# Kernel optimization log

Measured on AMD Instinct MI355X. Metric: run time of the kernel, lower is better.

Reference implementation:

```python
import jax, jax.numpy as jnp
import numpy as np

TOKEN = 40      # half window -> token_len D = 81
STRIDE = 4
NHEAD = 9
EPS = 1e-5
NEG = -1e30


def _tokenize(x):
    # x: [B, L] -> [B, S, D] centered sliding windows, zero padded
    B, L = x.shape
    D = 2 * TOKEN + 1
    S = -(-L // STRIDE)
    xp = jnp.pad(x, ((0, 0), (TOKEN, TOKEN)))
    idx = jnp.arange(S)[:, None] * STRIDE + jnp.arange(D)[None, :]
    return xp[:, idx]


def _pe(S, D):
    pos = jnp.arange(S, dtype=jnp.float32)[:, None]
    div = jnp.exp(-jnp.log(jnp.float32(10000.0)) * jnp.arange(0, D, 2, dtype=jnp.float32) / D)
    ang = pos * div  # [S, ceil(D/2)]
    pe = jnp.zeros((S, D), dtype=jnp.float32)
    pe = pe.at[:, 0::2].set(jnp.sin(ang))
    pe = pe.at[:, 1::2].set(jnp.cos(ang[:, : D // 2]))
    return pe


def _bn(x, g, b, axes):
    # training-mode batch norm over `axes`, channels last
    m = x.mean(axes, keepdims=True)
    v = x.var(axes, keepdims=True)
    return (x - m) / jnp.sqrt(v + EPS) * g + b


def _forward(x, basel, cali_spec, Wq, Wk, Wq2, Wk2, Wv2, Cv, Wo1, Wo2,
             corr_weight, h_weight, corr_map, g1, b1, ff1_w, ff1_b, g2, b2,
             ff2_w, ff2_b, g3, b3, token_v_w, token_v_b, beta1, alpha1, alpha2,
             fc1_w, fc1_b, bnf1_g, bnf1_b, fc2_w, fc2_b, bnf2_g, bnf2_b, fc3_w, fc3_b):
    D = 2 * TOKEN + 1
    dk = D // NHEAD
    # data normalization (load_data_scale semantics)
    xm = jnp.min(x[:, 20:-20])
    xs = jnp.abs(jnp.max(x[:, 20:-20] - xm))
    xn = (x - xm) / xs
    bs = basel[:, ::STRIDE]                      # [B, S]
    tx = _tokenize(xn)                           # [B, S, D]
    B, S, _ = tx.shape
    pe = _pe(S, D)
    tx = tx + pe
    cn = (cali_spec - xm) / xs
    tc = _tokenize(cn) + pe                      # [Bc, S, D]
    Bc = tc.shape[0]

    # ---- branch 2: calibration-spectrum attention over the batch dim ----
    Q2 = jnp.einsum('bse,hed->shbd', tx, Wq2)    # [S,H,B,dk]
    K2 = jnp.einsum('bse,hed->shbd', tx, Wk2)
    V2 = jnp.einsum('bse,hed->shbd', tx, Wv2)
    cK = jnp.einsum('cse,hed->shcd', tc, Wk2)    # [S,H,Bc,dk]
    cV = jnp.einsum('cse,hed->shcd', tc, Wv2)
    Kc = jnp.concatenate([K2, cK], axis=2)       # [S,H,B+Bc,dk]
    Vc = jnp.concatenate([V2, cV], axis=2)
    sc = jnp.einsum('shbd,shkd->shbk', Q2, Kc) / jnp.sqrt(jnp.float32(dk))
    cols = jnp.arange(B + Bc)
    # banded mask: each sample sees only itself among batch columns, all cali columns
    mask = (cols[None, :] >= B) | (cols[None, :] == jnp.arange(B)[:, None])  # [B, B+Bc]
    sc = jnp.where(mask[None, None], sc, NEG)
    A2 = jax.nn.softmax(sc, axis=-1)
    h2 = jnp.einsum('shbk,shkd->bshd', A2, Vc).reshape(B, S, D) @ Wo2  # [B,S,D]

    # ---- branch 1: correlation-map-biased attention over spectral positions ----
    xh = tx + h2
    Qs = jnp.einsum('bse,hed->bhsd', xh, Wq)
    Ks = jnp.einsum('bse,hed->bhsd', xh, Wk)
    Vs = jnp.einsum('bse,hed->bhsd', xh, Wq)     # original uses Wq for V (bug preserved)
    cw = corr_weight[0]
    bias = (corr_map @ Cv) / jnp.sqrt(jnp.float32(S))  # band_num == S
    As = (1.0 - cw) * jnp.einsum('bhsd,bhtd->bhst', Qs, Ks) / jnp.sqrt(jnp.float32(dk)) + cw * bias
    As = jax.nn.softmax(As, axis=-1)
    h1 = jnp.einsum('bhst,bhtd->bshd', As, Vs).reshape(B, S, D) @ Wo1
    hw = h_weight[0]
    att = (1.0 - hw) * h1 + hw * h2

    # ---- SpectrA residual + FF (BatchNorm over channels) ----
    ma = _bn(att + tx, g1, b1, (0, 1))
    f = jax.nn.relu(ma @ ff1_w + ff1_b)
    f = _bn(f, g2, b2, (0, 1))
    f = jax.nn.relu(f @ ff2_w + ff2_b)
    res = _bn(ma + f, g3, b3, (0, 1))

    # ---- ACiNet head ----
    a = (res @ token_v_w + token_v_b) * jax.nn.softmax(res @ beta1, axis=-1)
    a = a.sum(-1)                                # [B, S]
    fea = alpha1[0] * a + alpha2[0] * bs
    h = jax.nn.relu(fea @ fc1_w + fc1_b)
    h = _bn(h, bnf1_g, bnf1_b, (0,))
    h = jax.nn.relu(h @ fc2_w + fc2_b)
    h = _bn(h, bnf2_g, bnf2_b, (0,))
    return jnp.tanh(h @ fc3_w + fc3_b)


def setup_inputs() -> dict:
    key = jax.random.key(0)
    ks = iter(jax.random.split(key, 64))
    def rn(shape, s=0.05):
        return jax.random.normal(next(ks), shape, dtype=jnp.float32) * s
    B, Bc, L = 32, 16, 2048
    D, H, dk, S, FF, FC1, FC2, Y = 81, 9, 9, 512, 256, 512, 256, 4
    f32 = jnp.float32
    return {
        'x': rn((B, L), 1.0), 'basel': rn((B, L), 1.0), 'cali_spec': rn((Bc, L), 1.0),
        'Wq': rn((H, D, dk)), 'Wk': rn((H, D, dk)), 'Wq2': rn((H, D, dk)),
        'Wk2': rn((H, D, dk)), 'Wv2': rn((H, D, dk)),
        'Cv': rn((S, S)), 'Wo1': rn((D, D)), 'Wo2': rn((D, D)),
        'corr_weight': jnp.array([0.2], dtype=f32), 'h_weight': jnp.array([0.8], dtype=f32),
        'corr_map': rn((S, S), 1.0),
        'g1': jnp.ones(D, f32), 'b1': jnp.zeros(D, f32),
        'ff1_w': rn((D, FF)), 'ff1_b': jnp.zeros(FF, f32),
        'g2': jnp.ones(FF, f32), 'b2': jnp.zeros(FF, f32),
        'ff2_w': rn((FF, D)), 'ff2_b': jnp.zeros(D, f32),
        'g3': jnp.ones(D, f32), 'b3': jnp.zeros(D, f32),
        'token_v_w': rn((D, D)), 'token_v_b': jnp.zeros(D, f32),
        'beta1': jnp.ones((D, D), f32),
        'alpha1': jnp.array([0.8], dtype=f32), 'alpha2': jnp.array([0.2], dtype=f32),
        'fc1_w': rn((S, FC1)), 'fc1_b': jnp.zeros(FC1, f32),
        'bnf1_g': jnp.ones(FC1, f32), 'bnf1_b': jnp.zeros(FC1, f32),
        'fc2_w': rn((FC1, FC2)), 'fc2_b': jnp.zeros(FC2, f32),
        'bnf2_g': jnp.ones(FC2, f32), 'bnf2_b': jnp.zeros(FC2, f32),
        'fc3_w': rn((FC2, Y)), 'fc3_b': jnp.zeros(Y, f32),
    }


def reference(x, basel, cali_spec, Wq, Wk, Wq2, Wk2, Wv2, Cv, Wo1, Wo2,
              corr_weight, h_weight, corr_map, g1, b1, ff1_w, ff1_b, g2, b2,
              ff2_w, ff2_b, g3, b3, token_v_w, token_v_b, beta1, alpha1, alpha2,
              fc1_w, fc1_b, bnf1_g, bnf1_b, fc2_w, fc2_b, bnf2_g, bnf2_b, fc3_w, fc3_b):
    return _forward(x, basel, cali_spec, Wq, Wk, Wq2, Wk2, Wv2, Cv, Wo1, Wo2,
                    corr_weight, h_weight, corr_map, g1, b1, ff1_w, ff1_b, g2, b2,
                    ff2_w, ff2_b, g3, b3, token_v_w, token_v_b, beta1, alpha1, alpha2,
                    fc1_w, fc1_b, bnf1_g, bnf1_b, fc2_w, fc2_b, bnf2_g, bnf2_b, fc3_w, fc3_b)
```

## Files before the change

kernel.cpp:

```cpp
#include <hip/hip_runtime.h>
#include <hip/hip_bf16.h>
#include <math.h>

#define EPSV 1e-5f

typedef float vf4 __attribute__((ext_vector_type(4)));


__global__ void minmax_part(const float* __restrict__ x, float* __restrict__ part) {
    __shared__ float smin[256], smax[256];
    int tid = threadIdx.x;
    float mn = 1e30f, mx = -1e30f;
    for (int i = blockIdx.x * 256 + tid; i < 32 * 2008; i += 64 * 256) {
        int b = i / 2008, c = i % 2008 + 20;
        float v = x[b * 2048 + c];
        mn = fminf(mn, v); mx = fmaxf(mx, v);
    }
    smin[tid] = mn; smax[tid] = mx; __syncthreads();
    for (int off = 128; off > 0; off >>= 1) {
        if (tid < off) { smin[tid] = fminf(smin[tid], smin[tid + off]); smax[tid] = fmaxf(smax[tid], smax[tid + off]); }
        __syncthreads();
    }
    if (tid == 0) { part[blockIdx.x] = smin[0]; part[64 + blockIdx.x] = smax[0]; }
}

__global__ void minmax_fin(const float* __restrict__ part, float* __restrict__ scal) {
    __shared__ float smn[64], smx[64];
    int tid = threadIdx.x;
    smn[tid] = part[tid]; smx[tid] = part[64 + tid]; __syncthreads();
    for (int off = 32; off > 0; off >>= 1) {
        if (tid < off) { smn[tid] = fminf(smn[tid], smn[tid + off]); smx[tid] = fmaxf(smx[tid], smx[tid + off]); }
        __syncthreads();
    }
    if (tid == 0) { scal[0] = smn[0]; scal[1] = smx[0] - smn[0]; }
}

__global__ void pe_kernel(float* __restrict__ pe) {
    int idx = blockIdx.x * blockDim.x + threadIdx.x;
    if (idx >= 512 * 81) return;
    int d = idx % 81, s = idx / 81;
    int j = d >> 1;
    float dv = __expf(-9.210340371976184f * (2.0f * (float)j) / 81.0f);
    float ang = (float)s * dv;
    pe[idx] = (d & 1) ? cosf(ang) : sinf(ang);
}

__global__ void tokenize_kernel(const float* __restrict__ x, const float* __restrict__ cali,
                                const float* __restrict__ scal, const float* __restrict__ pe,
                                float* __restrict__ txall) {
    int idx = blockIdx.x * blockDim.x + threadIdx.x;
    if (idx >= 48 * 512 * 81) return;
    int d = idx % 81;
    int s = (idx / 81) % 512;
    int r = idx / (81 * 512);
    float xm = scal[0], inv_xs = 1.0f / scal[1];
    int oc = s * 4 + d - 40;
    float val = 0.0f;
    if (oc >= 0 && oc < 2048) {
        float sv = (r < 32) ? x[r * 2048 + oc] : cali[(r - 32) * 2048 + oc];
        val = (sv - xm) * inv_xs;
    }
    txall[idx] = val + pe[s * 81 + d];
}


__global__ __launch_bounds__(256) void qkv2_kernel(const float* __restrict__ txall,
                            const float* __restrict__ Wq2, const float* __restrict__ Wk2,
                            const float* __restrict__ Wv2,
                            float* __restrict__ Q2, float* __restrict__ Kc, float* __restrict__ Vc) {
    __shared__ float rows_[64 * 84];
    __shared__ float Wl[84 * 84];
    int blk = blockIdx.x;
    int t, rb;
    if (blk < 256)      { t = 0; rb = blk; }
    else if (blk < 640) { t = 1; rb = blk - 256; }
    else                { t = 2; rb = blk - 640; }
    int row0 = rb * 64;
    int k = row0 >> 9;
    int s0 = row0 & 511;
    const float* W = (t == 0) ? Wq2 : (t == 1) ? Wk2 : Wv2;
    int tid = threadIdx.x;
    for (int i = tid; i < 64 * 84; i += 256) {
        int c = i % 84;
        rows_[i] = (c < 81) ? txall[(row0 + i / 84) * 81 + c] : 0.0f;
    }
    for (int i = tid; i < 84 * 84; i += 256) {
        int e = i / 84, hd = i % 84;
        Wl[i] = (e < 81 && hd < 81) ? W[(hd / 9) * 729 + e * 9 + (hd % 9)] : 0.0f;
    }
    __syncthreads();
    for (int o = tid; o < 336; o += 256) {
        int r4 = o / 21, cg = o % 21;
        int c0 = cg * 4;
        const float* rp = rows_ + r4 * 4 * 84;
        vf4 acc0 = 0.0f, acc1 = 0.0f, acc2 = 0.0f, acc3 = 0.0f;
        #pragma unroll 7
        for (int e = 0; e < 84; e += 4) {
            vf4 w0 = *(const vf4*)(Wl + (e + 0) * 84 + c0);
            vf4 w1 = *(const vf4*)(Wl + (e + 1) * 84 + c0);
            vf4 w2 = *(const vf4*)(Wl + (e + 2) * 84 + c0);
            vf4 w3 = *(const vf4*)(Wl + (e + 3) * 84 + c0);
            vf4 r0 = *(const vf4*)(rp + e);
            vf4 r1 = *(const vf4*)(rp + 84 + e);
            vf4 r2 = *(const vf4*)(rp + 168 + e);
            vf4 r3 = *(const vf4*)(rp + 252 + e);
            acc0 += r0[0] * w0 + r0[1] * w1 + r0[2] * w2 + r0[3] * w3;
            acc1 += r1[0] * w0 + r1[1] * w1 + r1[2] * w2 + r1[3] * w3;
            acc2 += r2[0] * w0 + r2[1] * w1 + r2[2] * w2 + r2[3] * w3;
            acc3 += r3[0] * w0 + r3[1] * w1 + r3[2] * w2 + r3[3] * w3;
        }
        vf4 av[4] = {acc0, acc1, acc2, acc3};
        #pragma unroll
        for (int cc = 0; cc < 4; cc++) {
            int col = c0 + cc;
            if (col < 81) {
                int h = col / 9, d = col % 9;
                #pragma unroll
                for (int rr = 0; rr < 4; rr++) {
                    int s = s0 + r4 * 4 + rr;
                    if (t == 0)      Q2[((s * 9 + h) * 32 + k) * 9 + d] = av[rr][cc];
                    else if (t == 1) Kc[((s * 9 + h) * 48 + k) * 9 + d] = av[rr][cc];
                    else             Vc[((s * 9 + h) * 48 + k) * 9 + d] = av[rr][cc];
                }
            }
        }
    }
}

__global__ void attn2_kernel(const float* __restrict__ Q2, const float* __restrict__ Kc,
                             const float* __restrict__ Vc, float* __restrict__ tmp2) {
    int tid = blockIdx.x * blockDim.x + threadIdx.x;
    if (tid >= 512 * 9 * 32) return;
    int b = tid & 31;
    int h = (tid >> 5) % 9;
    int s = tid / 288;
    const float* q = Q2 + ((s * 9 + h) * 32 + b) * 9;
    float qr[9];
    #pragma unroll
    for (int d = 0; d < 9; d++) qr[d] = q[d] * (1.0f / 3.0f);
    const float* Kb = Kc + (s * 9 + h) * 48 * 9;
    const float* Vb = Vc + (s * 9 + h) * 48 * 9;
    float l = 0.0f, outv[9];
    #pragma unroll
    for (int d = 0; d < 9; d++) outv[d] = 0.0f;
    #pragma unroll
    for (int j = 0; j < 17; j++) {
        int k = (j == 0) ? b : 31 + j;
        const float* kp = Kb + k * 9;
        float acc = 0.0f;
        #pragma unroll
        for (int d = 0; d < 9; d++) acc += qr[d] * kp[d];
        float p = __expf(acc);
        l += p;
        const float* vp = Vb + k * 9;
        #pragma unroll
        for (int d = 0; d < 9; d++) outv[d] += p * vp[d];
    }
    float invl = 1.0f / l;
    float* op = tmp2 + (b * 512 + s) * 81 + h * 9;
    #pragma unroll
    for (int d = 0; d < 9; d++) op[d] = outv[d] * invl;
}

__global__ __launch_bounds__(256) void h2xh_kernel(const float* __restrict__ tmp2,
                            const float* __restrict__ Wo2, const float* __restrict__ txall,
                            float* __restrict__ h2, float* __restrict__ xh) {
    __shared__ float rows_[64 * 84];
    __shared__ float Wl[84 * 84];
    int row0 = blockIdx.x * 64;
    int tid = threadIdx.x;
    for (int i = tid; i < 64 * 84; i += 256) {
        int c = i % 84;
        rows_[i] = (c < 81) ? tmp2[(row0 + i / 84) * 81 + c] : 0.0f;
    }
    for (int i = tid; i < 84 * 84; i += 256) {
        int e = i / 84, c = i % 84;
        Wl[i] = (e < 81 && c < 81) ? Wo2[e * 81 + c] : 0.0f;
    }
    __syncthreads();
    for (int o = tid; o < 336; o += 256) {
        int r4 = o / 21, cg = o % 21;
        int c0 = cg * 4;
        const float* rp = rows_ + r4 * 4 * 84;
        vf4 acc0 = 0.0f, acc1 = 0.0f, acc2 = 0.0f, acc3 = 0.0f;
        #pragma unroll 7
        for (int e = 0; e < 84; e += 4) {
            vf4 w0 = *(const vf4*)(Wl + (e + 0) * 84 + c0);
            vf4 w1 = *(const vf4*)(Wl + (e + 1) * 84 + c0);
            vf4 w2 = *(const vf4*)(Wl + (e + 2) * 84 + c0);
            vf4 w3 = *(const vf4*)(Wl + (e + 3) * 84 + c0);
            vf4 r0 = *(const vf4*)(rp + e);
            vf4 r1 = *(const vf4*)(rp + 84 + e);
            vf4 r2 = *(const vf4*)(rp + 168 + e);
            vf4 r3 = *(const vf4*)(rp + 252 + e);
            acc0 += r0[0] * w0 + r0[1] * w1 + r0[2] * w2 + r0[3] * w3;
            acc1 += r1[0] * w0 + r1[1] * w1 + r1[2] * w2 + r1[3] * w3;
            acc2 += r2[0] * w0 + r2[1] * w1 + r2[2] * w2 + r2[3] * w3;
            acc3 += r3[0] * w0 + r3[1] * w1 + r3[2] * w2 + r3[3] * w3;
        }
        vf4 av[4] = {acc0, acc1, acc2, acc3};
        #pragma unroll
        for (int cc = 0; cc < 4; cc++) {
            int col = c0 + cc;
            if (col < 81) {
                #pragma unroll
                for (int rr = 0; rr < 4; rr++) {
                    int idx = (row0 + r4 * 4 + rr) * 81 + col;
                    float v = av[rr][cc];
                    h2[idx] = v;
                    xh[idx] = txall[idx] + v;
                }
            }
        }
    }
}

__global__ __launch_bounds__(256) void qks_kernel(const float* __restrict__ xh,
                           const float* __restrict__ Wq, const float* __restrict__ Wk,
                           float* __restrict__ Qs, float* __restrict__ Ks) {
    __shared__ float rows_[64 * 84];
    __shared__ float Wl[84 * 84];
    int blk = blockIdx.x;
    int t = blk >> 8;
    int rb = blk & 255;
    int row0 = rb * 64;
    int b = row0 >> 9;
    int s0 = row0 & 511;
    const float* W = (t == 0) ? Wq : Wk;
    int tid = threadIdx.x;
    for (int i = tid; i < 64 * 84; i += 256) {
        int c = i % 84;
        rows_[i] = (c < 81) ? xh[(row0 + i / 84) * 81 + c] : 0.0f;
    }
    for (int i = tid; i < 84 * 84; i += 256) {
        int e = i / 84, hd = i % 84;
        Wl[i] = (e < 81 && hd < 81) ? W[(hd / 9) * 729 + e * 9 + (hd % 9)] : 0.0f;
    }
    __syncthreads();
    float* dst = (t == 0) ? Qs : Ks;
    for (int o = tid; o < 336; o += 256) {
        int r4 = o / 21, cg = o % 21;
        int c0 = cg * 4;
        const float* rp = rows_ + r4 * 4 * 84;
        vf4 acc0 = 0.0f, acc1 = 0.0f, acc2 = 0.0f, acc3 = 0.0f;
        #pragma unroll 7
        for (int e = 0; e < 84; e += 4) {
            vf4 w0 = *(const vf4*)(Wl + (e + 0) * 84 + c0);
            vf4 w1 = *(const vf4*)(Wl + (e + 1) * 84 + c0);
            vf4 w2 = *(const vf4*)(Wl + (e + 2) * 84 + c0);
            vf4 w3 = *(const vf4*)(Wl + (e + 3) * 84 + c0);
            vf4 r0 = *(const vf4*)(rp + e);
            vf4 r1 = *(const vf4*)(rp + 84 + e);
            vf4 r2 = *(const vf4*)(rp + 168 + e);
            vf4 r3 = *(const vf4*)(rp + 252 + e);
            acc0 += r0[0] * w0 + r0[1] * w1 + r0[2] * w2 + r0[3] * w3;
            acc1 += r1[0] * w0 + r1[1] * w1 + r1[2] * w2 + r1[3] * w3;
            acc2 += r2[0] * w0 + r2[1] * w1 + r2[2] * w2 + r2[3] * w3;
            acc3 += r3[0] * w0 + r3[1] * w1 + r3[2] * w2 + r3[3] * w3;
        }
        vf4 av[4] = {acc0, acc1, acc2, acc3};
        #pragma unroll
        for (int cc = 0; cc < 4; cc++) {
            int col = c0 + cc;
            if (col < 81) {
                int h = col / 9, d = col % 9;
                #pragma unroll
                for (int rr = 0; rr < 4; rr++)
                    dst[((b * 9 + h) * 512 + (s0 + r4 * 4 + rr)) * 9 + d] = av[rr][cc];
            }
        }
    }
}

__global__ __launch_bounds__(256) void biasmm_kernel(const float* __restrict__ corr,
                              const float* __restrict__ Cv, const float* __restrict__ cwp,
                              float* __restrict__ ebT) {
    __shared__ float As[32][33];
    __shared__ float Bs[32][33];
    int tx = threadIdx.x, ty = threadIdx.y;
    int tid = ty * 16 + tx;
    int t0 = blockIdx.y * 32, s0 = blockIdx.x * 32;
    float a00 = 0, a01 = 0, a10 = 0, a11 = 0;
    for (int k0 = 0; k0 < 512; k0 += 32) {
        for (int ii = tid; ii < 1024; ii += 256) {
            int r = ii >> 5, c = ii & 31;
            As[r][c] = Cv[(k0 + r) * 512 + t0 + c];
            Bs[r][c] = corr[(s0 + r) * 512 + k0 + c];
        }
        __syncthreads();
        #pragma unroll
        for (int kk = 0; kk < 32; kk++) {
            float b0 = Bs[tx][kk], b1 = Bs[tx + 16][kk];
            float c0 = As[kk][ty], c1 = As[kk][ty + 16];
            a00 += c0 * b0; a01 += c0 * b1; a10 += c1 * b0; a11 += c1 * b1;
        }
        __syncthreads();
    }
    float cws = cwp[0] * 0.04419417382415922f;
    ebT[(t0 + ty) * 512 + s0 + tx]            = __expf(a00 * cws);
    ebT[(t0 + ty) * 512 + s0 + tx + 16]       = __expf(a01 * cws);
    ebT[(t0 + ty + 16) * 512 + s0 + tx]       = __expf(a10 * cws);
    ebT[(t0 + ty + 16) * 512 + s0 + tx + 16]  = __expf(a11 * cws);
}

__global__ __launch_bounds__(256) void attn1_kernel(const float* __restrict__ Qs,
                                                    const float* __restrict__ Ks,
                                                    const float* __restrict__ ebT,
                                                    const float* __restrict__ cwp,
                                                    float* __restrict__ part) {
    int blk = blockIdx.x;
    int bh = blk >> 2;
    int qhalf = (blk >> 1) & 1;
    int kq = blk & 1;
    int tid = threadIdx.x;
    const float* Kb = Ks + bh * 4608;
    const float* Qb = Qs + bh * 4608;
    int q = qhalf * 256 + tid;
    float c1 = (1.0f - cwp[0]) / 3.0f;
    float qv[9];
    {
        const float* qp = Qb + q * 9;
        #pragma unroll
        for (int d = 0; d < 9; d++) qv[d] = c1 * qp[d];
    }
    float l = 0.0f, acc[9];
    #pragma unroll
    for (int d = 0; d < 9; d++) acc[d] = 0.0f;
    int k0 = kq * 256;
    const float* ebp = ebT + q;
    #pragma unroll 4
    for (int t = k0; t < k0 + 256; t++) {
        const float* kr = Kb + t * 9;
        const float* vr = Qb + t * 9;
        float u = qv[0] * kr[0] + qv[1] * kr[1] + qv[2] * kr[2] + qv[3] * kr[3]
                + qv[4] * kr[4] + qv[5] * kr[5] + qv[6] * kr[6] + qv[7] * kr[7]
                + qv[8] * kr[8];
        float p = __expf(u) * ebp[t << 9];
        l += p;
        #pragma unroll
        for (int d = 0; d < 9; d++) acc[d] += p * vr[d];
    }
    float* pp = part + (size_t)kq * 1474560;
    int gidx = bh * 512 + q;
    pp[gidx] = l;
    #pragma unroll
    for (int e = 0; e < 9; e++) pp[(1 + e) * 147456 + gidx] = acc[e];
}

__global__ void attn1_merge(const float* __restrict__ part, float* __restrict__ h1tmp) {
    int idx = blockIdx.x * 256 + threadIdx.x;
    if (idx >= 147456) return;
    const float* p0 = part + idx;
    const float* p1 = part + 1474560 + idx;
    float L = p0[0] + p1[0];
    float invl = 1.0f / L;
    int bh = idx >> 9, q = idx & 511;
    int b = bh / 9, h = bh % 9;
    float* op = h1tmp + (b * 512 + q) * 81 + h * 9;
    #pragma unroll
    for (int d = 0; d < 9; d++)
        op[d] = (p0[(1 + d) * 147456] + p1[(1 + d) * 147456]) * invl;
}

__global__ __launch_bounds__(256) void h1o_kernel(const float* __restrict__ h1tmp,
                           const float* __restrict__ Wo1, const float* __restrict__ h2,
                           const float* __restrict__ txall, const float* __restrict__ hwp,
                           float* __restrict__ matin, float* __restrict__ st1) {
    __shared__ float rows_[64 * 84];
    __shared__ float Wl[84 * 84];
    __shared__ float ssum[81], ssq[81];
    int row0 = blockIdx.x * 64;
    int tid = threadIdx.x;
    if (tid < 81) { ssum[tid] = 0.0f; ssq[tid] = 0.0f; }
    for (int i = tid; i < 64 * 84; i += 256) {
        int c = i % 84;
        rows_[i] = (c < 81) ? h1tmp[(row0 + i / 84) * 81 + c] : 0.0f;
    }
    for (int i = tid; i < 84 * 84; i += 256) {
        int e = i / 84, c = i % 84;
        Wl[i] = (e < 81 && c < 81) ? Wo1[e * 81 + c] : 0.0f;
    }
    __syncthreads();
    float hw = hwp[0];
    float onemhw = 1.0f - hw;
    for (int o = tid; o < 336; o += 256) {
        int r4 = o / 21, cg = o % 21;
        int c0 = cg * 4;
        const float* rp = rows_ + r4 * 4 * 84;
        vf4 acc0 = 0.0f, acc1 = 0.0f, acc2 = 0.0f, acc3 = 0.0f;
        #pragma unroll 7
        for (int e = 0; e < 84; e += 4) {
            vf4 w0 = *(const vf4*)(Wl + (e + 0) * 84 + c0);
            vf4 w1 = *(const vf4*)(Wl + (e + 1) * 84 + c0);
            vf4 w2 = *(const vf4*)(Wl + (e + 2) * 84 + c0);
            vf4 w3 = *(const vf4*)(Wl + (e + 3) * 84 + c0);
            vf4 r0 = *(const vf4*)(rp + e);
            vf4 r1 = *(const vf4*)(rp + 84 + e);
            vf4 r2 = *(const vf4*)(rp + 168 + e);
            vf4 r3 = *(const vf4*)(rp + 252 + e);
            acc0 += r0[0] * w0 + r0[1] * w1 + r0[2] * w2 + r0[3] * w3;
            acc1 += r1[0] * w0 + r1[1] * w1 + r1[2] * w2 + r1[3] * w3;
            acc2 += r2[0] * w0 + r2[1] * w1 + r2[2] * w2 + r2[3] * w3;
            acc3 += r3[0] * w0 + r3[1] * w1 + r3[2] * w2 + r3[3] * w3;
        }
        vf4 av[4] = {acc0, acc1, acc2, acc3};
        #pragma unroll
        for (int cc = 0; cc < 4; cc++) {
            int col = c0 + cc;
            if (col < 81) {
                float ls = 0.0f, lq = 0.0f;
                #pragma unroll
                for (int rr = 0; rr < 4; rr++) {
                    int idx = (row0 + r4 * 4 + rr) * 81 + col;
                    float v = onemhw * av[rr][cc] + hw * h2[idx] + txall[idx];
                    matin[idx] = v;
                    ls += v; lq += v * v;
                }
                atomicAdd(&ssum[col], ls);
                atomicAdd(&ssq[col], lq);
            }
        }
    }
    __syncthreads();
    if (tid < 81) {
        atomicAdd(&st1[tid], ssum[tid]);
        atomicAdd(&st1[81 + tid], ssq[tid]);
    }
}

__global__ __launch_bounds__(256) void ff1_kernel(const float* __restrict__ matin,
                           const float* __restrict__ st1, const float* __restrict__ g1,
                           const float* __restrict__ b1, const float* __restrict__ W,
                           const float* __restrict__ bias, float* __restrict__ f1,
                           float* __restrict__ st2) {
    __shared__ float rows_[64 * 84];
    __shared__ float Wl[84 * 64];
    __shared__ float s2s[64], s2q[64];
    int row0 = blockIdx.x * 64;
    int cb = blockIdx.y * 64;
    int tid = threadIdx.x;
    const float invN = 1.0f / 16384.0f;
    if (tid < 64) { s2s[tid] = 0.0f; s2q[tid] = 0.0f; }
    for (int i = tid; i < 64 * 84; i += 256) {
        int c = i % 84;
        float v = 0.0f;
        if (c < 81) {
            float mean = st1[c] * invN;
            float var = st1[81 + c] * invN - mean * mean;
            v = (matin[(row0 + i / 84) * 81 + c] - mean) * rsqrtf(var + EPSV) * g1[c] + b1[c];
        }
        rows_[i] = v;
    }
    for (int i = tid; i < 84 * 64; i += 256) {
        int e = i >> 6, cc = i & 63;
        Wl[i] = (e < 81) ? W[e * 256 + cb + cc] : 0.0f;
    }
    __syncthreads();
    {
        int o = tid;
        int r4 = o >> 4, cg = o & 15;
        int c0 = cg * 4;
        const float* rp = rows_ + r4 * 4 * 84;
        vf4 acc0 = 0.0f, acc1 = 0.0f, acc2 = 0.0f, acc3 = 0.0f;
        #pragma unroll 7
        for (int e = 0; e < 84; e += 4) {
            vf4 w0 = *(const vf4*)(Wl + ((e + 0) << 6) + c0);
            vf4 w1 = *(const vf4*)(Wl + ((e + 1) << 6) + c0);
            vf4 w2 = *(const vf4*)(Wl + ((e + 2) << 6) + c0);
            vf4 w3 = *(const vf4*)(Wl + ((e + 3) << 6) + c0);
            vf4 r0 = *(const vf4*)(rp + e);
            vf4 r1 = *(const vf4*)(rp + 84 + e);
            vf4 r2 = *(const vf4*)(rp + 168 + e);
            vf4 r3 = *(const vf4*)(rp + 252 + e);
            acc0 += r0[0] * w0 + r0[1] * w1 + r0[2] * w2 + r0[3] * w3;
            acc1 += r1[0] * w0 + r1[1] * w1 + r1[2] * w2 + r1[3] * w3;
            acc2 += r2[0] * w0 + r2[1] * w1 + r2[2] * w2 + r2[3] * w3;
            acc3 += r3[0] * w0 + r3[1] * w1 + r3[2] * w2 + r3[3] * w3;
        }
        vf4 bv = *(const vf4*)(bias + cb + c0);
        acc0 = __builtin_elementwise_max(acc0 + bv, (vf4)0.0f);
        acc1 = __builtin_elementwise_max(acc1 + bv, (vf4)0.0f);
        acc2 = __builtin_elementwise_max(acc2 + bv, (vf4)0.0f);
        acc3 = __builtin_elementwise_max(acc3 + bv, (vf4)0.0f);
        int base = (row0 + r4 * 4) * 256 + cb + c0;
        *(vf4*)(f1 + base)       = acc0;
        *(vf4*)(f1 + base + 256) = acc1;
        *(vf4*)(f1 + base + 512) = acc2;
        *(vf4*)(f1 + base + 768) = acc3;
        vf4 cs = acc0 + acc1 + acc2 + acc3;
        vf4 cq = acc0 * acc0 + acc1 * acc1 + acc2 * acc2 + acc3 * acc3;
        #pragma unroll
        for (int cc = 0; cc < 4; cc++) {
            atomicAdd(&s2s[c0 + cc], cs[cc]);
            atomicAdd(&s2q[c0 + cc], cq[cc]);
        }
    }
    __syncthreads();
    if (tid < 64) {
        atomicAdd(&st2[cb + tid], s2s[tid]);
        atomicAdd(&st2[256 + cb + tid], s2q[tid]);
    }
}

__global__ __launch_bounds__(256) void ff2_kernel(const float* __restrict__ f1,
                           const float* __restrict__ st2, const float* __restrict__ g2,
                           const float* __restrict__ b2, const float* __restrict__ W,
                           const float* __restrict__ bias, const float* __restrict__ matin,
                           const float* __restrict__ st1, const float* __restrict__ g1,
                           const float* __restrict__ b1, float* __restrict__ t3,
                           float* __restrict__ st3) {
    __shared__ float rows_[32 * 64];
    __shared__ float Wl[64 * 84];
    __shared__ float s3s[81], s3q[81];
    int row0 = blockIdx.x * 32;
    int tid = threadIdx.x;
    const float invN = 1.0f / 16384.0f;
    if (tid < 81) { s3s[tid] = 0.0f; s3q[tid] = 0.0f; }
    int o = tid;
    int r4 = o / 21, cg = o % 21;
    int c0 = cg * 4;
    bool active = (o < 168);
    vf4 acc0 = 0.0f, acc1 = 0.0f, acc2 = 0.0f, acc3 = 0.0f;
    for (int kq = 0; kq < 4; kq++) {
        __syncthreads();
        for (int i = tid; i < 32 * 64; i += 256) {
            int r = i >> 6, e = i & 63;
            int c = kq * 64 + e;
            float mean = st2[c] * invN;
            float var = st2[256 + c] * invN - mean * mean;
            rows_[i] = (f1[(row0 + r) * 256 + c] - mean) * rsqrtf(var + EPSV) * g2[c] + b2[c];
        }
        for (int i = tid; i < 64 * 84; i += 256) {
            int e = i / 84, c = i % 84;
            Wl[i] = (c < 81) ? W[(kq * 64 + e) * 81 + c] : 0.0f;
        }
        __syncthreads();
        if (active) {
            const float* rp = rows_ + r4 * 4 * 64;
            #pragma unroll 8
            for (int e = 0; e < 64; e += 4) {
                vf4 w0 = *(const vf4*)(Wl + (e + 0) * 84 + c0);
                vf4 w1 = *(const vf4*)(Wl + (e + 1) * 84 + c0);
                vf4 w2 = *(const vf4*)(Wl + (e + 2) * 84 + c0);
                vf4 w3 = *(const vf4*)(Wl + (e + 3) * 84 + c0);
                vf4 r0 = *(const vf4*)(rp + e);
                vf4 r1 = *(const vf4*)(rp + 64 + e);
                vf4 r2 = *(const vf4*)(rp + 128 + e);
                vf4 r3 = *(const vf4*)(rp + 192 + e);
                acc0 += r0[0] * w0 + r0[1] * w1 + r0[2] * w2 + r0[3] * w3;
                acc1 += r1[0] * w0 + r1[1] * w1 + r1[2] * w2 + r1[3] * w3;
                acc2 += r2[0] * w0 + r2[1] * w1 + r2[2] * w2 + r2[3] * w3;
                acc3 += r3[0] * w0 + r3[1] * w1 + r3[2] * w2 + r3[3] * w3;
            }
        }
    }
    if (active) {
        vf4 av[4] = {acc0, acc1, acc2, acc3};
        #pragma unroll
        for (int cc = 0; cc < 4; cc++) {
            int col = c0 + cc;
            if (col < 81) {
                float mean = st1[col] * invN;
                float var = st1[81 + col] * invN - mean * mean;
                float rstd = rsqrtf(var + EPSV);
                float bval = bias[col];
                float ls = 0.0f, lq = 0.0f;
                #pragma unroll
                for (int rr = 0; rr < 4; rr++) {
                    int idx = (row0 + r4 * 4 + rr) * 81 + col;
                    float ma = (matin[idx] - mean) * rstd * g1[col] + b1[col];
                    float v = ma + fmaxf(av[rr][cc] + bval, 0.0f);
                    t3[idx] = v;
                    ls += v; lq += v * v;
                }
                atomicAdd(&s3s[col], ls);
                atomicAdd(&s3q[col], lq);
            }
        }
    }
    __syncthreads();
    if (tid < 81) {
        atomicAdd(&st3[tid], s3s[tid]);
        atomicAdd(&st3[81 + tid], s3q[tid]);
    }
}

__global__ __launch_bounds__(256) void token_mm(const float* __restrict__ t3,
                            const float* __restrict__ st3, const float* __restrict__ g3,
                            const float* __restrict__ b3, const float* __restrict__ tvw,
                            const float* __restrict__ beta1,
                            float* __restrict__ uv0, float* __restrict__ uv1) {
    __shared__ float rows_[64 * 84];
    __shared__ float Wl[84 * 84];
    int blk = blockIdx.x;
    int t = blk >> 8;
    int row0 = (blk & 255) * 64;
    const float* W = (t == 0) ? tvw : beta1;
    float* dst = (t == 0) ? uv0 : uv1;
    int tid = threadIdx.x;
    const float invN = 1.0f / 16384.0f;
    for (int i = tid; i < 64 * 84; i += 256) {
        int c = i % 84;
        float v = 0.0f;
        if (c < 81) {
            float mean = st3[c] * invN;
            float var = st3[81 + c] * invN - mean * mean;
            v = (t3[(row0 + i / 84) * 81 + c] - mean) * rsqrtf(var + EPSV) * g3[c] + b3[c];
        }
        rows_[i] = v;
    }
    for (int i = tid; i < 84 * 84; i += 256) {
        int e = i / 84, c = i % 84;
        Wl[i] = (e < 81 && c < 81) ? W[e * 81 + c] : 0.0f;
    }
    __syncthreads();
    for (int o = tid; o < 336; o += 256) {
        int r4 = o / 21, cg = o % 21;
        int c0 = cg * 4;
        const float* rp = rows_ + r4 * 4 * 84;
        vf4 acc0 = 0.0f, acc1 = 0.0f, acc2 = 0.0f, acc3 = 0.0f;
        #pragma unroll 7
        for (int e = 0; e < 84; e += 4) {
            vf4 w0 = *(const vf4*)(Wl + (e + 0) * 84 + c0);
            vf4 w1 = *(const vf4*)(Wl + (e + 1) * 84 + c0);
            vf4 w2 = *(const vf4*)(Wl + (e + 2) * 84 + c0);
            vf4 w3 = *(const vf4*)(Wl + (e + 3) * 84 + c0);
            vf4 r0 = *(const vf4*)(rp + e);
            vf4 r1 = *(const vf4*)(rp + 84 + e);
            vf4 r2 = *(const vf4*)(rp + 168 + e);
            vf4 r3 = *(const vf4*)(rp + 252 + e);
            acc0 += r0[0] * w0 + r0[1] * w1 + r0[2] * w2 + r0[3] * w3;
            acc1 += r1[0] * w0 + r1[1] * w1 + r1[2] * w2 + r1[3] * w3;
            acc2 += r2[0] * w0 + r2[1] * w1 + r2[2] * w2 + r2[3] * w3;
            acc3 += r3[0] * w0 + r3[1] * w1 + r3[2] * w2 + r3[3] * w3;
        }
        vf4 av[4] = {acc0, acc1, acc2, acc3};
        #pragma unroll
        for (int cc = 0; cc < 4; cc++) {
            int col = c0 + cc;
            if (col < 81) {
                #pragma unroll
                for (int rr = 0; rr < 4; rr++)
                    dst[(row0 + r4 * 4 + rr) * 81 + col] = av[rr][cc];
            }
        }
    }
}

__global__ __launch_bounds__(256) void token_pool(const float* __restrict__ uv0,
                             const float* __restrict__ uv1, const float* __restrict__ tvb,
                             const float* __restrict__ basel, const float* __restrict__ a1p,
                             const float* __restrict__ a2p, float* __restrict__ fea) {
    int tid = threadIdx.x;
    int r = tid >> 3, j = tid & 7;
    int row = blockIdx.x * 32 + r;
    int base = row * 81;
    float u[11], v[11];
    #pragma unroll
    for (int dd = 0; dd < 11; dd++) {
        int d = j + dd * 8;
        if (d < 81) {
            u[dd] = uv0[base + d] + tvb[d];
            v[dd] = uv1[base + d];
        } else {
            u[dd] = 0.0f; v[dd] = -1e30f;
        }
    }
    float mx = -1e30f;
    #pragma unroll
    for (int dd = 0; dd < 11; dd++) mx = fmaxf(mx, v[dd]);
    #pragma unroll
    for (int msk = 1; msk < 8; msk <<= 1) mx = fmaxf(mx, __shfl_xor(mx, msk, 8));
    float sp = 0.0f, sup = 0.0f;
    #pragma unroll
    for (int dd = 0; dd < 11; dd++) {
        float p = __expf(v[dd] - mx);
        sp += p; sup += u[dd] * p;
    }
    #pragma unroll
    for (int msk = 1; msk < 8; msk <<= 1) {
        sp  += __shfl_xor(sp, msk, 8);
        sup += __shfl_xor(sup, msk, 8);
    }
    if (j == 0) {
        int b = row >> 9, s = row & 511;
        fea[row] = a1p[0] * (sup / sp) + a2p[0] * basel[b * 2048 + s * 4];
    }
}

__global__ void fc1_kernel(const float* __restrict__ in, const float* __restrict__ W,
                           const float* __restrict__ bias, float* __restrict__ out,
                           float* __restrict__ st) {
    int idx = blockIdx.x * blockDim.x + threadIdx.x;
    if (idx >= 32 * 512) return;
    int b = idx >> 9, j = idx & 511;
    float acc = bias[j];
    const float* ip = in + (b << 9);
    #pragma unroll 8
    for (int k = 0; k < 512; k++) acc += ip[k] * W[k * 512 + j];
    acc = fmaxf(acc, 0.0f);
    out[idx] = acc;
    atomicAdd(&st[j], acc);
    atomicAdd(&st[512 + j], acc * acc);
}

__global__ __launch_bounds__(256) void fc2_kernel(const float* __restrict__ in,
                           const float* __restrict__ st4, const float* __restrict__ g,
                           const float* __restrict__ bb, const float* __restrict__ W,
                           const float* __restrict__ bias, float* __restrict__ out,
                           float* __restrict__ st5) {
    __shared__ float scale[512], shift[512];
    int tid = threadIdx.x;
    for (int k = tid; k < 512; k += 256) {
        float mean = st4[k] * (1.0f / 32.0f);
        float var = st4[512 + k] * (1.0f / 32.0f) - mean * mean;
        float sc_ = rsqrtf(var + EPSV) * g[k];
        scale[k] = sc_;
        shift[k] = bb[k] - mean * sc_;
    }
    __syncthreads();
    int idx = blockIdx.x * 256 + tid;
    if (idx >= 32 * 256) return;
    int b = idx >> 8, j = idx & 255;
    float acc = bias[j];
    const float* ip = in + (b << 9);
    #pragma unroll 8
    for (int k = 0; k < 512; k++) acc += (ip[k] * scale[k] + shift[k]) * W[k * 256 + j];
    acc = fmaxf(acc, 0.0f);
    out[idx] = acc;
    atomicAdd(&st5[j], acc);
    atomicAdd(&st5[256 + j], acc * acc);
}

__global__ void fc3_kernel(const float* __restrict__ in, const float* __restrict__ st5,
                           const float* __restrict__ g, const float* __restrict__ bb,
                           const float* __restrict__ W, const float* __restrict__ bias,
                           float* __restrict__ out) {
    __shared__ float scale[256], shift[256];
    int tid = threadIdx.x;
    for (int k = tid; k < 256; k += 128) {
        float mean = st5[k] * (1.0f / 32.0f);
        float var = st5[256 + k] * (1.0f / 32.0f) - mean * mean;
        float sc_ = rsqrtf(var + EPSV) * g[k];
        scale[k] = sc_;
        shift[k] = bb[k] - mean * sc_;
    }
    __syncthreads();
    int b = tid >> 2, j = tid & 3;
    float acc = bias[j];
    const float* ip = in + (b << 8);
    #pragma unroll 8
    for (int k = 0; k < 256; k++) acc += (ip[k] * scale[k] + shift[k]) * W[k * 4 + j];
    out[tid] = tanhf(acc);
}

extern "C" void kernel_launch(void* const* d_in, const int* in_sizes, int n_in,
                              void* d_out, int out_size, void* d_ws, size_t ws_size,
                              hipStream_t stream) {
    const float* x       = (const float*)d_in[0];
    const float* basel   = (const float*)d_in[1];
    const float* cali    = (const float*)d_in[2];
    const float* Wq      = (const float*)d_in[3];
    const float* Wk      = (const float*)d_in[4];
    const float* Wq2     = (const float*)d_in[5];
    const float* Wk2     = (const float*)d_in[6];
    const float* Wv2     = (const float*)d_in[7];
    const float* Cv      = (const float*)d_in[8];
    const float* Wo1     = (const float*)d_in[9];
    const float* Wo2     = (const float*)d_in[10];
    const float* corr_w  = (const float*)d_in[11];
    const float* h_w     = (const float*)d_in[12];
    const float* corr    = (const float*)d_in[13];
    const float* g1      = (const float*)d_in[14];
    const float* b1      = (const float*)d_in[15];
    const float* ff1_w   = (const float*)d_in[16];
    const float* ff1_b   = (const float*)d_in[17];
    const float* g2      = (const float*)d_in[18];
    const float* b2      = (const float*)d_in[19];
    const float* ff2_w   = (const float*)d_in[20];
    const float* ff2_b   = (const float*)d_in[21];
    const float* g3      = (const float*)d_in[22];
    const float* b3      = (const float*)d_in[23];
    const float* tvw     = (const float*)d_in[24];
    const float* tvb     = (const float*)d_in[25];
    const float* beta1   = (const float*)d_in[26];
    const float* a1      = (const float*)d_in[27];
    const float* a2      = (const float*)d_in[28];
    const float* fc1_w   = (const float*)d_in[29];
    const float* fc1_b   = (const float*)d_in[30];
    const float* bnf1_g  = (const float*)d_in[31];
    const float* bnf1_b  = (const float*)d_in[32];
    const float* fc2_w   = (const float*)d_in[33];
    const float* fc2_b   = (const float*)d_in[34];
    const float* bnf2_g  = (const float*)d_in[35];
    const float* bnf2_b  = (const float*)d_in[36];
    const float* fc3_w   = (const float*)d_in[37];
    const float* fc3_b   = (const float*)d_in[38];
    float* out = (float*)d_out;
    float* ws = (float*)d_ws;

    const size_t SCAL  = 0;
    const size_t PART  = 16;
    const size_t ST1   = 512;
    const size_t ST2   = 768;
    const size_t ST3   = 1536;
    const size_t ST4   = 1792;
    const size_t ST5   = 2880;
    const size_t FEA   = 4096;
    const size_t FCH1  = 20480;
    const size_t FCH2  = 36864;
    const size_t PEO   = 45056;
    const size_t TX    = 90112;
    const size_t Q2O   = 2080768;
    const size_t KCO   = 3407872;
    const size_t VCO   = 5398528;
    const size_t TMP2  = 7389184;
    const size_t H2O   = 8716288;
    const size_t XHO   = 10043392;
    const size_t BIASO = 11370496;
    const size_t F1O   = 11632640;

    float* scal  = ws + SCAL;
    float* part  = ws + PART;
    float* st1   = ws + ST1;
    float* st2   = ws + ST2;
    float* st3   = ws + ST3;
    float* st4   = ws + ST4;
    float* st5   = ws + ST5;
    float* fea   = ws + FEA;
    float* fch1  = ws + FCH1;
    float* fch2  = ws + FCH2;
    float* pe    = ws + PEO;
    float* txall = ws + TX;
    float* Q2    = ws + Q2O;
    float* Kc    = ws + KCO;
    float* Vc    = ws + VCO;
    float* tmp2  = ws + TMP2;
    float* h2    = ws + H2O;
    float* xh    = ws + XHO;
    float* ebT   = ws + BIASO;
    float* f1    = ws + F1O;
    float* h1tmp = Q2;
    float* Qs    = Kc;
    float* Ks    = Vc;
    float* matin = tmp2;
    float* t3    = h2;
    float* apart = f1;
    float* uv0   = tmp2;
    float* uv1   = xh;

    hipMemsetAsync(ws, 0, 4096 * sizeof(float), stream);

    minmax_part<<<64, 256, 0, stream>>>(x, part);
    minmax_fin<<<1, 64, 0, stream>>>(part, scal);

    pe_kernel<<<(512 * 81 + 255) / 256, 256, 0, stream>>>(pe);

    tokenize_kernel<<<(48 * 512 * 81 + 255) / 256, 256, 0, stream>>>(x, cali, scal, pe, txall);

    qkv2_kernel<<<1024, 256, 0, stream>>>(txall, Wq2, Wk2, Wv2, Q2, Kc, Vc);

    attn2_kernel<<<(512 * 9 * 32) / 256, 256, 0, stream>>>(Q2, Kc, Vc, tmp2);

    h2xh_kernel<<<256, 256, 0, stream>>>(tmp2, Wo2, txall, h2, xh);

    qks_kernel<<<512, 256, 0, stream>>>(xh, Wq, Wk, Qs, Ks);

    biasmm_kernel<<<dim3(16, 16), dim3(16, 16), 0, stream>>>(corr, Cv, corr_w, ebT);

    attn1_kernel<<<1152, 256, 0, stream>>>(Qs, Ks, ebT, corr_w, apart);
    attn1_merge<<<576, 256, 0, stream>>>(apart, h1tmp);

    h1o_kernel<<<256, 256, 0, stream>>>(h1tmp, Wo1, h2, txall, h_w, matin, st1);

    ff1_kernel<<<dim3(256, 4), 256, 0, stream>>>(matin, st1, g1, b1, ff1_w, ff1_b, f1, st2);

    ff2_kernel<<<512, 256, 0, stream>>>(f1, st2, g2, b2, ff2_w, ff2_b,
                                        matin, st1, g1, b1, t3, st3);

    token_mm<<<512, 256, 0, stream>>>(t3, st3, g3, b3, tvw, beta1, uv0, uv1);
    token_pool<<<512, 256, 0, stream>>>(uv0, uv1, tvb, basel, a1, a2, fea);

    fc1_kernel<<<64, 256, 0, stream>>>(fea, fc1_w, fc1_b, fch1, st4);

    fc2_kernel<<<32, 256, 0, stream>>>(fch1, st4, bnf1_g, bnf1_b, fc2_w, fc2_b, fch2, st5);

    fc3_kernel<<<1, 128, 0, stream>>>(fch2, st5, bnf2_g, bnf2_b, fc3_w, fc3_b, out);
}
```

Measured before the change: 483.9 us.

## Fuse attention split-merge into output projection, use exp2 and packed float2 math

The separate merge kernel for the split-key attention partials is removed, and the output-projection kernel now reads both partial sums directly while building its shared-memory rows. This saves one launch and one intermediate buffer round trip. Softmax exponentials switch to exp2f, with log2(e) folded into the query scale. The attention inner loop is rewritten with float2 vectors so the compiler can emit packed FMA instructions. The fused load does a division per element and reads strided partials, which may be less coalesced.

```diff
diff --git a/kernel.cpp b/kernel.cpp
--- a/kernel.cpp
+++ b/kernel.cpp
@@ -4,6 +4,7 @@
 
 #define EPSV 1e-5f
 
+typedef float vf2 __attribute__((ext_vector_type(2)));
 typedef float vf4 __attribute__((ext_vector_type(4)));
 
 
@@ -136,8 +137,9 @@
     int s = tid / 288;
     const float* q = Q2 + ((s * 9 + h) * 32 + b) * 9;
     float qr[9];
-    #pragma unroll
-    for (int d = 0; d < 9; d++) qr[d] = q[d] * (1.0f / 3.0f);
+    const float c2 = 1.4426950408889634f / 3.0f;
+    #pragma unroll
+    for (int d = 0; d < 9; d++) qr[d] = q[d] * c2;
     const float* Kb = Kc + (s * 9 + h) * 48 * 9;
     const float* Vb = Vc + (s * 9 + h) * 48 * 9;
     float l = 0.0f, outv[9];
@@ -150,7 +152,7 @@
         float acc = 0.0f;
         #pragma unroll
         for (int d = 0; d < 9; d++) acc += qr[d] * kp[d];
-        float p = __expf(acc);
+        float p = exp2f(acc);
         l += p;
         const float* vp = Vb + k * 9;
         #pragma unroll
@@ -316,53 +318,57 @@
     const float* Kb = Ks + bh * 4608;
     const float* Qb = Qs + bh * 4608;
     int q = qhalf * 256 + tid;
-    float c1 = (1.0f - cwp[0]) / 3.0f;
-    float qv[9];
+    float c1 = (1.0f - cwp[0]) * (1.4426950408889634f / 3.0f);
+    vf2 qv[4];
+    float q8;
     {
         const float* qp = Qb + q * 9;
         #pragma unroll
-        for (int d = 0; d < 9; d++) qv[d] = c1 * qp[d];
-    }
-    float l = 0.0f, acc[9];
-    #pragma unroll
-    for (int d = 0; d < 9; d++) acc[d] = 0.0f;
+        for (int d = 0; d < 4; d++) {
+            vf2 t; t.x = c1 * qp[2 * d]; t.y = c1 * qp[2 * d + 1];
+            qv[d] = t;
+        }
+        q8 = c1 * qp[8];
+    }
+    float l = 0.0f, a8 = 0.0f;
+    vf2 acc[4];
+    #pragma unroll
+    for (int d = 0; d < 4; d++) acc[d] = (vf2)0.0f;
     int k0 = kq * 256;
     const float* ebp = ebT + q;
     #pragma unroll 4
     for (int t = k0; t < k0 + 256; t++) {
         const float* kr = Kb + t * 9;
         const float* vr = Qb + t * 9;
-        float u = qv[0] * kr[0] + qv[1] * kr[1] + qv[2] * kr[2] + qv[3] * kr[3]
-                + qv[4] * kr[4] + qv[5] * kr[5] + qv[6] * kr[6] + qv[7] * kr[7]
-                + qv[8] * kr[8];
-        float p = __expf(u) * ebp[t << 9];
+        vf2 k0v; k0v.x = kr[0]; k0v.y = kr[1];
+        vf2 k1v; k1v.x = kr[2]; k1v.y = kr[3];
+        vf2 k2v; k2v.x = kr[4]; k2v.y = kr[5];
+        vf2 k3v; k3v.x = kr[6]; k3v.y = kr[7];
+        vf2 u2 = qv[0] * k0v + qv[1] * k1v + qv[2] * k2v + qv[3] * k3v;
+        float u = u2.x + u2.y + q8 * kr[8];
+        float p = exp2f(u) * ebp[t << 9];
         l += p;
-        #pragma unroll
-        for (int d = 0; d < 9; d++) acc[d] += p * vr[d];
+        vf2 p2; p2.x = p; p2.y = p;
+        vf2 v0; v0.x = vr[0]; v0.y = vr[1];
+        vf2 v1; v1.x = vr[2]; v1.y = vr[3];
+        vf2 v2; v2.x = vr[4]; v2.y = vr[5];
+        vf2 v3; v3.x = vr[6]; v3.y = vr[7];
+        acc[0] += p2 * v0; acc[1] += p2 * v1;
+        acc[2] += p2 * v2; acc[3] += p2 * v3;
+        a8 += p * vr[8];
     }
     float* pp = part + (size_t)kq * 1474560;
     int gidx = bh * 512 + q;
     pp[gidx] = l;
     #pragma unroll
-    for (int e = 0; e < 9; e++) pp[(1 + e) * 147456 + gidx] = acc[e];
-}
-
-__global__ void attn1_merge(const float* __restrict__ part, float* __restrict__ h1tmp) {
-    int idx = blockIdx.x * 256 + threadIdx.x;
-    if (idx >= 147456) return;
-    const float* p0 = part + idx;
-    const float* p1 = part + 1474560 + idx;
-    float L = p0[0] + p1[0];
-    float invl = 1.0f / L;
-    int bh = idx >> 9, q = idx & 511;
-    int b = bh / 9, h = bh % 9;
-    float* op = h1tmp + (b * 512 + q) * 81 + h * 9;
-    #pragma unroll
-    for (int d = 0; d < 9; d++)
-        op[d] = (p0[(1 + d) * 147456] + p1[(1 + d) * 147456]) * invl;
-}
-
-__global__ __launch_bounds__(256) void h1o_kernel(const float* __restrict__ h1tmp,
+    for (int d = 0; d < 4; d++) {
+        pp[(1 + 2 * d) * 147456 + gidx] = acc[d].x;
+        pp[(2 + 2 * d) * 147456 + gidx] = acc[d].y;
+    }
+    pp[9 * 147456 + gidx] = a8;
+}
+
+__global__ __launch_bounds__(256) void h1o_kernel(const float* __restrict__ apart,
                            const float* __restrict__ Wo1, const float* __restrict__ h2,
                            const float* __restrict__ txall, const float* __restrict__ hwp,
                            float* __restrict__ matin, float* __restrict__ st1) {
@@ -373,8 +379,19 @@
     int tid = threadIdx.x;
     if (tid < 81) { ssum[tid] = 0.0f; ssq[tid] = 0.0f; }
     for (int i = tid; i < 64 * 84; i += 256) {
-        int c = i % 84;
-        rows_[i] = (c < 81) ? h1tmp[(row0 + i / 84) * 81 + c] : 0.0f;
+        int r = i / 84, c = i % 84;
+        float v = 0.0f;
+        if (c < 81) {
+            int row = row0 + r;
+            int b = row >> 9, s = row & 511;
+            int h = c / 9, d = c % 9;
+            int gidx = (b * 9 + h) * 512 + s;
+            float L = apart[gidx] + apart[1474560 + gidx];
+            float A = apart[(1 + d) * 147456 + gidx]
+                    + apart[1474560 + (1 + d) * 147456 + gidx];
+            v = A / L;
+        }
+        rows_[i] = v;
     }
     for (int i = tid; i < 84 * 84; i += 256) {
         int e = i / 84, c = i % 84;
@@ -840,7 +857,6 @@
     float* xh    = ws + XHO;
     float* ebT   = ws + BIASO;
     float* f1    = ws + F1O;
-    float* h1tmp = Q2;
     float* Qs    = Kc;
     float* Ks    = Vc;
     float* matin = tmp2;
@@ -869,9 +885,8 @@
     biasmm_kernel<<<dim3(16, 16), dim3(16, 16), 0, stream>>>(corr, Cv, corr_w, ebT);
 
     attn1_kernel<<<1152, 256, 0, stream>>>(Qs, Ks, ebT, corr_w, apart);
-    attn1_merge<<<576, 256, 0, stream>>>(apart, h1tmp);
-
-    h1o_kernel<<<256, 256, 0, stream>>>(h1tmp, Wo1, h2, txall, h_w, matin, st1);
+
+    h1o_kernel<<<256, 256, 0, stream>>>(apart, Wo1, h2, txall, h_w, matin, st1);
 
     ff1_kernel<<<dim3(256, 4), 256, 0, stream>>>(matin, st1, g1, b1, ff1_w, ff1_b, f1, st2);
 
```

After: 479.2 us. No clear change (-1.0%).
